# Kernel tuning notes

Hardware: AMD Instinct MI355X
Metric: run time of the kernel (lower is better)

## Reference

```python
import jax, jax.numpy as jnp
import numpy as np

N_NODES = 50000   # n_nodes (adjacency is [N,N])
NNZ = 800000      # nonzeros per support (avg degree 16)
S = 3             # number of supports
D_IN = 512
D_OUT = 256


def setup_inputs() -> dict:
    key = jax.random.key(0)
    k0, k1, k2, k3, k4, k5 = jax.random.split(key, 6)
    x = jax.random.normal(k0, (N_NODES, D_IN), dtype=jnp.float32)
    # glorot-uniform per-support weights, stacked [S, D_IN, D_OUT]
    scale = float(np.sqrt(6.0 / (D_IN + D_OUT)))
    W = jax.random.uniform(k1, (S, D_IN, D_OUT), dtype=jnp.float32, minval=-scale, maxval=scale)
    rows = jax.random.randint(k2, (S, NNZ), 0, N_NODES, dtype=jnp.int32)
    cols = jax.random.randint(k3, (S, NNZ), 0, N_NODES, dtype=jnp.int32)
    vals = jax.random.uniform(k4, (S, NNZ), dtype=jnp.float32)
    # Conv1d(in=S, out=1, k=1, bias=False) == learned weighted sum over supports
    cw = jax.random.normal(k5, (S,), dtype=jnp.float32) * 0.5
    return {"x": x, "W": W, "rows": rows, "cols": cols, "vals": vals, "cw": cw}


def reference(x, W, rows, cols, vals, cw):
    # mod='output': out = relu( sum_i cw[i] * (A_i @ (x @ W_i)) )
    def spmm(r, c, v, pre):
        # A in COO: out[r] += v * pre[c]
        msgs = v[:, None] * pre[c]          # [NNZ, D_OUT] gather
        return jax.ops.segment_sum(msgs, r, num_segments=N_NODES)

    out = jnp.zeros((N_NODES, D_OUT), dtype=x.dtype)
    for i in range(S):                      # small fixed support count
        pre = x @ W[i]                      # dense GEMM [N, D_OUT]
        out = out + cw[i] * spmm(rows[i], cols[i], vals[i], pre)
    return jax.nn.relu(out)
```

## Files before the change

### kernel.cpp

```cpp
#include <hip/hip_runtime.h>
#include <stdint.h>

#define N_NODES 50000
#define N_PAD   50048
#define NNZ     800000
#define SUP     3
#define D_IN    512
#define D_OUT   256
#define TOT_E   (SUP * NNZ)
#define NBUCK   391
#define CAP     6976
#define CHUNK   6144
#define NB_WPREP 1536
#define NB_XPREP 12500
#define NB_GEMM  2346

typedef __attribute__((ext_vector_type(8))) short bf16x8;
typedef __attribute__((ext_vector_type(4))) float f32x4;
typedef __attribute__((address_space(3))) unsigned int lds_u32_t;
typedef const __attribute__((address_space(1))) unsigned int glb_u32_t;

static __device__ __forceinline__ unsigned short f2bf(float f) {
    unsigned int u = __float_as_uint(f);
    unsigned int r = (u + 0x7fffu + ((u >> 16) & 1u)) >> 16;
    return (unsigned short)r;
}
static __device__ __forceinline__ unsigned int pack_bf2(float lo, float hi) {
    unsigned int a = __float_as_uint(lo) + 0x8000u;
    unsigned int b = __float_as_uint(hi) + 0x8000u;
    return (a >> 16) | (b & 0xffff0000u);
}
static __device__ __forceinline__ float bf2f(unsigned short h) {
    return __uint_as_float(((unsigned int)h) << 16);
}

__global__ __launch_bounds__(256) void prep_kernel(const float* __restrict__ x,
                                                   unsigned int* __restrict__ xb,
                                                   const float* __restrict__ W,
                                                   unsigned short* __restrict__ Wt) {
    const int blk = blockIdx.x;
    const int tid = threadIdx.x;
    if (blk < NB_XPREP) {
        int idx = blk * 256 + tid;
        const f32x4* src = (const f32x4*)(x) + idx * 2;
        f32x4 f0 = __builtin_nontemporal_load(src);
        f32x4 f1 = __builtin_nontemporal_load(src + 1);
        uint4 o;
        o.x = pack_bf2(f0.x, f0.y);
        o.y = pack_bf2(f0.z, f0.w);
        o.z = pack_bf2(f1.x, f1.y);
        o.w = pack_bf2(f1.z, f1.w);
        *((uint4*)xb + idx) = o;
    } else {
        int idx = (blk - NB_XPREP) * 256 + tid;
        int n = idx & (D_OUT - 1);
        int k = (idx >> 8) & (D_IN - 1);
        int s = idx >> 17;
        Wt[((size_t)s * D_OUT + n) * D_IN + k] = f2bf(W[idx]);
    }
}

__global__ __launch_bounds__(256) void bucket_kernel(const int* __restrict__ rows,
                                                     const int* __restrict__ cols,
                                                     const float* __restrict__ vals,
                                                     const float* __restrict__ cw,
                                                     int* __restrict__ bucket_cursor,
                                                     int2* __restrict__ buck) {
    __shared__ double smem8[8590];
    char* smem = (char*)smem8;
    const int blk = blockIdx.x;
    const int tid = threadIdx.x;

    int2* stage = (int2*)smem;
    unsigned short* bucket_of = (unsigned short*)(smem + 49152);
    int* hist   = (int*)(smem + 61440);
    int* sc     = hist + NBUCK;
    int* sstart = sc + 256;
    int* lcur   = sstart + NBUCK;
    int* gbase  = lcur + NBUCK;

    const int base_n = blk * CHUNK;
    const int count = min(CHUNK, TOT_E - base_n);
    float cw0 = cw[0], cw1 = cw[1], cw2 = cw[2];

    for (int i = tid; i < NBUCK; i += 256) hist[i] = 0;
    __syncthreads();
    for (int i = tid; i < count; i += 256)
        atomicAdd(&hist[rows[base_n + i] >> 7], 1);
    __syncthreads();
    int b0 = 2 * tid, b1 = b0 + 1;
    int h0 = (b0 < NBUCK) ? hist[b0] : 0;
    int h1 = (b1 < NBUCK) ? hist[b1] : 0;
    sc[tid] = h0 + h1;
    __syncthreads();
    for (int off = 1; off < 256; off <<= 1) {
        int t = (tid >= off) ? sc[tid - off] : 0;
        __syncthreads();
        sc[tid] += t;
        __syncthreads();
    }
    int excl = sc[tid] - (h0 + h1);
    if (b0 < NBUCK) { sstart[b0] = excl;      lcur[b0] = excl; }
    if (b1 < NBUCK) { sstart[b1] = excl + h0; lcur[b1] = excl + h0; }
    for (int i = tid; i < NBUCK; i += 256)
        gbase[i] = atomicAdd(&bucket_cursor[i], hist[i]);
    __syncthreads();
    for (int i = tid; i < count; i += 256) {
        int n = base_n + i;
        int r = rows[n];
        int c = cols[n];
        float v = vals[n];
        int s = n / NNZ;
        float w = v * (s == 0 ? cw0 : (s == 1 ? cw1 : cw2));
        int b = r >> 7;
        int p = atomicAdd(&lcur[b], 1);
        stage[p] = make_int2(((r & 127) << 18) | (s * N_NODES + c), __float_as_int(w));
        bucket_of[p] = (unsigned short)b;
    }
    __syncthreads();
    for (int i = tid; i < count; i += 256) {
        int b = bucket_of[i];
        int local_off = i - sstart[b];
        buck[(size_t)b * CAP + gbase[b] + local_off] = stage[i];
    }
}

__global__ __launch_bounds__(256) void sort_kernel(const int2* __restrict__ buck,
                                                   const int* __restrict__ bucket_cursor,
                                                   int2* __restrict__ cv,
                                                   int* __restrict__ base,
                                                   int* __restrict__ cnt) {
    __shared__ double smem8[7232];
    char* smem = (char*)smem8;
    const int tid = threadIdx.x;

    int2* stage = (int2*)smem;
    int* hist   = (int*)(smem + 55808);
    int* sc     = hist + 128;
    int* sstart = sc + 128;
    int* cur    = sstart + 128;

    const int b = blockIdx.x;
    const int sz = bucket_cursor[b];
    const int2* src = buck + (size_t)b * CAP;

    if (tid < 128) hist[tid] = 0;
    __syncthreads();
    for (int i = tid; i < sz; i += 256)
        atomicAdd(&hist[((unsigned)src[i].x) >> 18], 1);
    __syncthreads();
    if (tid < 128) sc[tid] = hist[tid];
    __syncthreads();
    for (int off = 1; off < 128; off <<= 1) {
        int t = (tid >= off && tid < 128) ? sc[tid - off] : 0;
        __syncthreads();
        if (tid < 128) sc[tid] += t;
        __syncthreads();
    }
    if (tid < 128) {
        int st = sc[tid] - hist[tid];
        sstart[tid] = st;
        cur[tid] = st;
    }
    __syncthreads();
    for (int i = tid; i < sz; i += 256) {
        int2 e = src[i];
        int rl = ((unsigned)e.x) >> 18;
        int p = atomicAdd(&cur[rl], 1);
        stage[p] = make_int2(e.x & 0x3FFFF, e.y);
    }
    __syncthreads();
    size_t gb = (size_t)b * CAP;
    for (int i = tid; i < sz; i += 256) cv[gb + i] = stage[i];
    int r = b * 128 + tid;
    if (tid < 128 && r < N_NODES) {
        base[r] = (int)gb + sstart[tid];
        cnt[r]  = hist[tid];
    }
}

__global__ __launch_bounds__(256) void gemm_kernel(const unsigned short* __restrict__ xb,
                                                   const unsigned short* __restrict__ Wt,
                                                   unsigned short* __restrict__ pre) {
    __shared__ unsigned short lds_a[128 * 64];
    __shared__ unsigned short lds_b[128 * 64];
    const int blk = blockIdx.x;
    const int tid = threadIdx.x;

    constexpr int SWQ = NB_GEMM / 8;
    constexpr int SWR = NB_GEMM % 8;
    const int xcd = blk & 7, pos = blk >> 3;
    const int my = (xcd < SWR ? xcd * (SWQ + 1)
                              : SWR * (SWQ + 1) + (xcd - SWR) * SWQ) + pos;
    const int mt  = my / 6;
    const int rem = my % 6;
    const int m0 = mt * 128;
    const int n0 = (rem & 1) * 128;
    const int s  = rem >> 1;
    const unsigned short* wt = Wt + (size_t)s * D_OUT * D_IN;
    const int wave = tid >> 6;
    const int lane = tid & 63;
    const int quad = lane >> 4;
    const int lo   = lane & 15;
    const int wm = (wave & 1) * 64;
    const int wn = (wave >> 1) * 64;

    f32x4 acc[4][4] = {};

    for (int kb = 0; kb < D_IN; kb += 64) {
        __syncthreads();
        #pragma unroll
        for (int c = 0; c < 4; ++c) {
            int idx = c * 256 + tid;
            int row = idx >> 3;
            int kp  = idx & 7;
            const unsigned short* ga = xb + (size_t)(m0 + row) * D_IN + kb + kp * 8;
            __builtin_amdgcn_global_load_lds((glb_u32_t*)ga,
                                             (lds_u32_t*)&lds_a[idx * 8], 16, 0, 0);
            const unsigned short* gb = wt + (size_t)(n0 + row) * D_IN + kb + kp * 8;
            __builtin_amdgcn_global_load_lds((glb_u32_t*)gb,
                                             (lds_u32_t*)&lds_b[idx * 8], 16, 0, 0);
        }
        __syncthreads();

        #pragma unroll
        for (int t = 0; t < 2; ++t) {
            bf16x8 af[4], bfr[4];
            #pragma unroll
            for (int i = 0; i < 4; ++i)
                af[i] = *(const bf16x8*)&lds_a[(wm + 16 * i + lo) * 64 + t * 32 + quad * 8];
            #pragma unroll
            for (int j = 0; j < 4; ++j)
                bfr[j] = *(const bf16x8*)&lds_b[(wn + 16 * j + lo) * 64 + t * 32 + quad * 8];
            #pragma unroll
            for (int i = 0; i < 4; ++i)
                #pragma unroll
                for (int j = 0; j < 4; ++j)
                    acc[i][j] = __builtin_amdgcn_mfma_f32_16x16x32_bf16(af[i], bfr[j], acc[i][j], 0, 0, 0);
        }
    }

    #pragma unroll
    for (int i = 0; i < 4; ++i) {
        #pragma unroll
        for (int j = 0; j < 4; ++j) {
            int gn = n0 + wn + 16 * j + lo;
            #pragma unroll
            for (int r = 0; r < 4; ++r) {
                int gm2 = m0 + wm + 16 * i + quad * 4 + r;
                if (gm2 < N_NODES)
                    pre[((size_t)s * N_NODES + gm2) * D_OUT + gn] = f2bf(acc[i][j][r]);
            }
        }
    }
}

__global__ __launch_bounds__(256) void spmm_kernel(const unsigned short* __restrict__ pre,
                                                   const int* __restrict__ base,
                                                   const int* __restrict__ cnt,
                                                   const int2* __restrict__ cv,
                                                   float* __restrict__ out) {
    int row  = blockIdx.x * 4 + (threadIdx.x >> 6);
    int lane = threadIdx.x & 63;
    int start = base[row];
    int end   = start + cnt[row];
    float a0 = 0.f, a1 = 0.f, a2 = 0.f, a3 = 0.f;
    int j = start;
    for (; j + 8 <= end; j += 8) {
        int2 e[8];
        #pragma unroll
        for (int q = 0; q < 8; ++q) e[q] = cv[j + q];
        ushort4 p[8];
        #pragma unroll
        for (int q = 0; q < 8; ++q)
            p[q] = *(const ushort4*)(pre + (size_t)e[q].x * D_OUT + lane * 4);
        #pragma unroll
        for (int q = 0; q < 8; ++q) {
            float w = __int_as_float(e[q].y);
            a0 += w * bf2f(p[q].x);
            a1 += w * bf2f(p[q].y);
            a2 += w * bf2f(p[q].z);
            a3 += w * bf2f(p[q].w);
        }
    }
    for (; j + 4 <= end; j += 4) {
        int2 e[4];
        #pragma unroll
        for (int q = 0; q < 4; ++q) e[q] = cv[j + q];
        ushort4 p[4];
        #pragma unroll
        for (int q = 0; q < 4; ++q)
            p[q] = *(const ushort4*)(pre + (size_t)e[q].x * D_OUT + lane * 4);
        #pragma unroll
        for (int q = 0; q < 4; ++q) {
            float w = __int_as_float(e[q].y);
            a0 += w * bf2f(p[q].x);
            a1 += w * bf2f(p[q].y);
            a2 += w * bf2f(p[q].z);
            a3 += w * bf2f(p[q].w);
        }
    }
    for (; j < end; ++j) {
        int2 e = cv[j];
        float w = __int_as_float(e.y);
        ushort4 p = *(const ushort4*)(pre + (size_t)e.x * D_OUT + lane * 4);
        a0 += w * bf2f(p.x);
        a1 += w * bf2f(p.y);
        a2 += w * bf2f(p.z);
        a3 += w * bf2f(p.w);
    }
    float4 o = make_float4(fmaxf(a0, 0.f), fmaxf(a1, 0.f), fmaxf(a2, 0.f), fmaxf(a3, 0.f));
    *(float4*)(out + (size_t)row * D_OUT + lane * 4) = o;
}

extern "C" void kernel_launch(void* const* d_in, const int* in_sizes, int n_in,
                              void* d_out, int out_size, void* d_ws, size_t ws_size,
                              hipStream_t stream) {
    const float* x    = (const float*)d_in[0];
    const float* W    = (const float*)d_in[1];
    const int*   rows = (const int*)d_in[2];
    const int*   cols = (const int*)d_in[3];
    const float* vals = (const float*)d_in[4];
    const float* cw   = (const float*)d_in[5];
    float* out = (float*)d_out;

    char* ws = (char*)d_ws;
    size_t off = 0;
    auto alloc = [&](size_t bytes) -> void* {
        void* p = ws + off;
        off += (bytes + 255) & ~(size_t)255;
        return p;
    };
    unsigned short* pre  = (unsigned short*)alloc((size_t)SUP * N_NODES * D_OUT * 2);
    unsigned short* xb   = (unsigned short*)alloc((size_t)N_PAD * D_IN * 2);
    unsigned short* Wt   = (unsigned short*)alloc((size_t)SUP * D_OUT * D_IN * 2);
    int* base            = (int*)alloc((size_t)N_NODES * 4);
    int* cnt             = (int*)alloc((size_t)N_NODES * 4);
    int* bucket_cursor   = (int*)alloc((size_t)NBUCK * 4);
    int2* cv             = (int2*)alloc((size_t)NBUCK * CAP * 8);
    int2* buck           = (int2*)d_out;

    hipMemsetAsync(bucket_cursor, 0, (size_t)NBUCK * 4, stream);

    bucket_kernel<<<NBUCK, 256, 0, stream>>>(rows, cols, vals, cw, bucket_cursor, buck);
    prep_kernel<<<NB_XPREP + NB_WPREP, 256, 0, stream>>>(x, (unsigned int*)xb, W, Wt);
    sort_kernel<<<NBUCK, 256, 0, stream>>>(buck, bucket_cursor, cv, base, cnt);
    gemm_kernel<<<NB_GEMM, 256, 0, stream>>>(xb, Wt, pre);
    spmm_kernel<<<N_NODES / 4, 256, 0, stream>>>(pre, base, cnt, cv, out);
}
```

Before: 477.8 us.

## Sort edges by row and column sub-bin; halve bucket chunk; add nontemporal loads

The sort kernel now bins each row's edges by column range (37 bins of 4096 columns per row), so gathers from the pre matrix during SpMM walk memory in roughly ascending column order and get better cache locality. The bucket kernel processes half-size chunks over twice as many blocks to raise parallelism and cut LDS use. Nontemporal loads and stores are added for edge-list reads and output writes so streaming data does not evict the pre matrix from cache. The finer histogram adds scan work and more LDS use in the sort kernel.

```diff
diff --git a/kernel.cpp b/kernel.cpp
--- a/kernel.cpp
+++ b/kernel.cpp
@@ -10,7 +10,10 @@
 #define TOT_E   (SUP * NNZ)
 #define NBUCK   391
 #define CAP     6976
-#define CHUNK   6144
+#define CHUNK   3072
+#define NBB     782
+#define NCB     37
+#define NBIN    (128 * NCB)
 #define NB_WPREP 1536
 #define NB_XPREP 12500
 #define NB_GEMM  2346
@@ -32,6 +35,13 @@
 }
 static __device__ __forceinline__ float bf2f(unsigned short h) {
     return __uint_as_float(((unsigned int)h) << 16);
+}
+static __device__ __forceinline__ int2 ldnt_int2(const int2* p) {
+    long long v = __builtin_nontemporal_load((const long long*)p);
+    int2 r;
+    r.x = (int)(v & 0xffffffffLL);
+    r.y = (int)(v >> 32);
+    return r;
 }
 
 __global__ __launch_bounds__(256) void prep_kernel(const float* __restrict__ x,
@@ -66,14 +76,14 @@
                                                      const float* __restrict__ cw,
                                                      int* __restrict__ bucket_cursor,
                                                      int2* __restrict__ buck) {
-    __shared__ double smem8[8590];
+    __shared__ double smem8[4750];
     char* smem = (char*)smem8;
     const int blk = blockIdx.x;
     const int tid = threadIdx.x;
 
     int2* stage = (int2*)smem;
-    unsigned short* bucket_of = (unsigned short*)(smem + 49152);
-    int* hist   = (int*)(smem + 61440);
+    unsigned short* bucket_of = (unsigned short*)(smem + 24576);
+    int* hist   = (int*)(smem + 30720);
     int* sc     = hist + NBUCK;
     int* sstart = sc + 256;
     int* lcur   = sstart + NBUCK;
@@ -108,8 +118,8 @@
     for (int i = tid; i < count; i += 256) {
         int n = base_n + i;
         int r = rows[n];
-        int c = cols[n];
-        float v = vals[n];
+        int c = __builtin_nontemporal_load(&cols[n]);
+        float v = __builtin_nontemporal_load(&vals[n]);
         int s = n / NNZ;
         float w = v * (s == 0 ? cw0 : (s == 1 ? cw1 : cw2));
         int b = r >> 7;
@@ -130,52 +140,63 @@
                                                    int2* __restrict__ cv,
                                                    int* __restrict__ base,
                                                    int* __restrict__ cnt) {
-    __shared__ double smem8[7232];
+    __shared__ double smem8[9537];
     char* smem = (char*)smem8;
     const int tid = threadIdx.x;
 
-    int2* stage = (int2*)smem;
-    int* hist   = (int*)(smem + 55808);
-    int* sc     = hist + 128;
-    int* sstart = sc + 128;
-    int* cur    = sstart + 128;
+    int2* stage   = (int2*)smem;
+    int* hist     = (int*)(smem + 55808);
+    int* sc       = hist + NBIN;
+    int* rowstart = sc + 256;
 
     const int b = blockIdx.x;
     const int sz = bucket_cursor[b];
     const int2* src = buck + (size_t)b * CAP;
 
-    if (tid < 128) hist[tid] = 0;
-    __syncthreads();
-    for (int i = tid; i < sz; i += 256)
-        atomicAdd(&hist[((unsigned)src[i].x) >> 18], 1);
-    __syncthreads();
-    if (tid < 128) sc[tid] = hist[tid];
-    __syncthreads();
-    for (int off = 1; off < 128; off <<= 1) {
-        int t = (tid >= off && tid < 128) ? sc[tid - off] : 0;
-        __syncthreads();
-        if (tid < 128) sc[tid] += t;
-        __syncthreads();
-    }
-    if (tid < 128) {
-        int st = sc[tid] - hist[tid];
-        sstart[tid] = st;
-        cur[tid] = st;
-    }
+    for (int i = tid; i < NBIN; i += 256) hist[i] = 0;
+    __syncthreads();
+    for (int i = tid; i < sz; i += 256) {
+        int key = src[i].x;
+        int bin = (key >> 18) * NCB + ((key & 0x3FFFF) >> 12);
+        atomicAdd(&hist[bin], 1);
+    }
+    __syncthreads();
+    const int lo = tid * 19;
+    const int hi = min(lo + 19, NBIN);
+    int acc = 0;
+    for (int i = lo; i < hi; ++i) acc += hist[i];
+    sc[tid] = acc;
+    __syncthreads();
+    for (int off = 1; off < 256; off <<= 1) {
+        int t = (tid >= off) ? sc[tid - off] : 0;
+        __syncthreads();
+        sc[tid] += t;
+        __syncthreads();
+    }
+    int run = sc[tid] - acc;
+    for (int i = lo; i < hi; ++i) {
+        int h = hist[i];
+        hist[i] = run;
+        run += h;
+    }
+    __syncthreads();
+    if (tid < 128) rowstart[tid] = hist[tid * NCB];
+    if (tid == 0)  rowstart[128] = sz;
     __syncthreads();
     for (int i = tid; i < sz; i += 256) {
         int2 e = src[i];
-        int rl = ((unsigned)e.x) >> 18;
-        int p = atomicAdd(&cur[rl], 1);
-        stage[p] = make_int2(e.x & 0x3FFFF, e.y);
+        int key = e.x;
+        int bin = (key >> 18) * NCB + ((key & 0x3FFFF) >> 12);
+        int p = atomicAdd(&hist[bin], 1);
+        stage[p] = make_int2(key & 0x3FFFF, e.y);
     }
     __syncthreads();
     size_t gb = (size_t)b * CAP;
     for (int i = tid; i < sz; i += 256) cv[gb + i] = stage[i];
     int r = b * 128 + tid;
     if (tid < 128 && r < N_NODES) {
-        base[r] = (int)gb + sstart[tid];
-        cnt[r]  = hist[tid];
+        base[r] = (int)gb + rowstart[tid];
+        cnt[r]  = rowstart[tid + 1] - rowstart[tid];
     }
 }
 
@@ -269,7 +290,7 @@
     for (; j + 8 <= end; j += 8) {
         int2 e[8];
         #pragma unroll
-        for (int q = 0; q < 8; ++q) e[q] = cv[j + q];
+        for (int q = 0; q < 8; ++q) e[q] = ldnt_int2(&cv[j + q]);
         ushort4 p[8];
         #pragma unroll
         for (int q = 0; q < 8; ++q)
@@ -286,7 +307,7 @@
     for (; j + 4 <= end; j += 4) {
         int2 e[4];
         #pragma unroll
-        for (int q = 0; q < 4; ++q) e[q] = cv[j + q];
+        for (int q = 0; q < 4; ++q) e[q] = ldnt_int2(&cv[j + q]);
         ushort4 p[4];
         #pragma unroll
         for (int q = 0; q < 4; ++q)
@@ -301,7 +322,7 @@
         }
     }
     for (; j < end; ++j) {
-        int2 e = cv[j];
+        int2 e = ldnt_int2(&cv[j]);
         float w = __int_as_float(e.y);
         ushort4 p = *(const ushort4*)(pre + (size_t)e.x * D_OUT + lane * 4);
         a0 += w * bf2f(p.x);
@@ -309,8 +330,12 @@
         a2 += w * bf2f(p.z);
         a3 += w * bf2f(p.w);
     }
-    float4 o = make_float4(fmaxf(a0, 0.f), fmaxf(a1, 0.f), fmaxf(a2, 0.f), fmaxf(a3, 0.f));
-    *(float4*)(out + (size_t)row * D_OUT + lane * 4) = o;
+    f32x4 o;
+    o.x = fmaxf(a0, 0.f);
+    o.y = fmaxf(a1, 0.f);
+    o.z = fmaxf(a2, 0.f);
+    o.w = fmaxf(a3, 0.f);
+    __builtin_nontemporal_store(o, (f32x4*)(out + (size_t)row * D_OUT + lane * 4));
 }
 
 extern "C" void kernel_launch(void* const* d_in, const int* in_sizes, int n_in,
@@ -342,7 +367,7 @@
 
     hipMemsetAsync(bucket_cursor, 0, (size_t)NBUCK * 4, stream);
 
-    bucket_kernel<<<NBUCK, 256, 0, stream>>>(rows, cols, vals, cw, bucket_cursor, buck);
+    bucket_kernel<<<NBB, 256, 0, stream>>>(rows, cols, vals, cw, bucket_cursor, buck);
     prep_kernel<<<NB_XPREP + NB_WPREP, 256, 0, stream>>>(x, (unsigned int*)xb, W, Wt);
     sort_kernel<<<NBUCK, 256, 0, stream>>>(buck, bucket_cursor, cv, base, cnt);
     gemm_kernel<<<NB_GEMM, 256, 0, stream>>>(xb, Wt, pre);
```

Measured after the change: 481.4 us. About the same (+0.7%).
